# Optimization experiments

Measured on AMD Instinct MI355X. Metric: run time of the kernel, lower is better.

## Reference

```python
import jax, jax.numpy as jnp
import numpy as np
from jax import lax

P_COARSE, P_FINE = 8, 4
EMBED_DIM = 128


def _patchify(x, p):
    # torch unfold(kernel=p, stride=p) then transpose: [B, Hp*Wp, C*p*p]
    B, C, H, W = x.shape
    Hp, Wp = H // p, W // p
    t = x.reshape(B, C, Hp, p, Wp, p).transpose(0, 2, 4, 1, 3, 5)
    return t.reshape(B, Hp * Wp, C * p * p), Hp, Wp


def _edge_map(x):
    gray = x.mean(axis=1, keepdims=True)
    kx = jnp.array([[-1., 0., 1.], [-2., 0., 2.], [-1., 0., 1.]], gray.dtype)[None, None]
    ky = jnp.array([[-1., -2., -1.], [0., 0., 0.], [1., 2., 1.]], gray.dtype)[None, None]
    pad = [(1, 1), (1, 1)]
    sx = lax.conv_general_dilated(gray, kx, (1, 1), pad)
    sy = lax.conv_general_dilated(gray, ky, (1, 1), pad)
    e = jnp.sqrt(sx * sx + sy * sy)
    B, _, H, W = e.shape
    # avg_pool2d(4, stride=4)
    return e.reshape(B, 1, H // 4, 4, W // 4, 4).mean(axis=(3, 5))


def _compact(tok, m):
    # stream-compact masked rows to the front, zero-pad the rest (pad_sequence semantics, padded to full Nf)
    Nf, D = tok.shape
    pos = jnp.cumsum(m) - 1
    pos = jnp.where(m, pos, Nf)  # unmasked rows go to overflow slot
    out = jnp.zeros((Nf + 1, D), tok.dtype).at[pos].set(tok)
    return out[:Nf]


def setup_inputs() -> dict:
    key = jax.random.key(0)
    ks = jax.random.split(key, 6)
    D = EMBED_DIM
    pd_c = 1 * P_COARSE * P_COARSE
    pd_f = 1 * P_FINE * P_FINE
    return {
        "x": jax.random.normal(ks[0], (8, 1, 512, 512), jnp.float32),
        "w_coarse": jax.random.normal(ks[1], (pd_c, D), jnp.float32) / np.sqrt(pd_c),
        "b_coarse": jnp.zeros((D,), jnp.float32),
        "w_fine": jax.random.normal(ks[2], (pd_f, D), jnp.float32) / np.sqrt(pd_f),
        "b_fine": jnp.zeros((D,), jnp.float32),
        "type_emb": jax.random.normal(ks[3], (2, D), jnp.float32) * 0.02,
    }


def reference(x, w_coarse, b_coarse, w_fine, b_fine, type_emb):
    B = x.shape[0]
    # coarse branch
    pc, Hc, Wc = _patchify(x, P_COARSE)
    coarse = pc @ w_coarse + b_coarse + type_emb[0]  # [B, Nc, D]
    # edge-driven mask
    edges = _edge_map(x)  # [B,1,He,We]
    mask = edges > edges.mean(axis=(2, 3), keepdims=True)
    # fine branch
    pf, Hf, Wf = _patchify(x, P_FINE)
    fine = pf @ w_fine + b_fine  # [B, Nf, D]
    # nearest upsample mask to (Hf, Wf): integer factor repeat
    m = mask[:, 0]
    m = jnp.repeat(jnp.repeat(m, Hf // m.shape[1], axis=1), Wf // m.shape[2], axis=2)
    mask_flat = m.reshape(B, -1)  # [B, Nf]
    fine_c = jax.vmap(_compact)(fine, mask_flat) + type_emb[1]
    tokens = jnp.concatenate([coarse, fine_c], axis=1)
    return tokens, mask_flat
```

## Files before the change

kernel.cpp:

```cpp
#include <hip/hip_runtime.h>

#define IMH 512
#define IMW 512
#define BATCH 8
#define NTOK 20480
#define NC 4096
#define NF 16384
#define ED 128

__global__ __launch_bounds__(256) void edge_kernel(const float* __restrict__ x,
                                                   double* __restrict__ edges) {
    int b = blockIdx.z;
    int ty0 = blockIdx.y * 64;
    int tx0 = blockIdx.x * 64;
    __shared__ float sm[66][68];
    const float* img = x + (size_t)b * (IMH * IMW);
    for (int idx = threadIdx.x; idx < 66 * 66; idx += 256) {
        int r = idx / 66, c = idx - r * 66;
        int gy = ty0 - 1 + r, gx = tx0 - 1 + c;
        float v = 0.f;
        if (gy >= 0 && gy < IMH && gx >= 0 && gx < IMW) v = img[gy * IMW + gx];
        sm[r][c] = v;
    }
    __syncthreads();
    int t = threadIdx.x;
    int cy = t >> 4, cx = t & 15;
    double acc = 0.0;
    #pragma unroll
    for (int dy = 0; dy < 4; ++dy) {
        int py = cy * 4 + dy + 1;
        #pragma unroll
        for (int dx = 0; dx < 4; ++dx) {
            int px = cx * 4 + dx + 1;
            double a00 = (double)sm[py - 1][px - 1];
            double a01 = (double)sm[py - 1][px];
            double a02 = (double)sm[py - 1][px + 1];
            double a10 = (double)sm[py][px - 1];
            double a12 = (double)sm[py][px + 1];
            double a20 = (double)sm[py + 1][px - 1];
            double a21 = (double)sm[py + 1][px];
            double a22 = (double)sm[py + 1][px + 1];
            double sx = (a02 + 2.0 * a12 + a22) - (a00 + 2.0 * a10 + a20);
            double sy = (a20 + 2.0 * a21 + a22) - (a00 + 2.0 * a01 + a02);
            acc += sqrt(sx * sx + sy * sy);
        }
    }
    int gy = (ty0 >> 2) + cy;
    int gx = (tx0 >> 2) + cx;
    edges[((size_t)b << 14) + gy * 128 + gx] = acc * (1.0 / 16.0);
}

__global__ __launch_bounds__(1024) void scan_kernel(const double* __restrict__ edges,
                                                    int* __restrict__ pos,
                                                    int* __restrict__ Karr,
                                                    float* __restrict__ mask_out) {
    int b = blockIdx.x;
    const double* e = edges + ((size_t)b << 14);
    int t = threadIdx.x;
    double v[16];
    double s = 0.0;
    #pragma unroll
    for (int j = 0; j < 16; ++j) { v[j] = e[t * 16 + j]; s += v[j]; }
    __shared__ double red[1024];
    red[t] = s;
    __syncthreads();
    for (int off = 512; off > 0; off >>= 1) {
        if (t < off) red[t] += red[t + off];
        __syncthreads();
    }
    double mean = red[0] * (1.0 / 16384.0);
    int m[16];
    int cnt = 0;
    #pragma unroll
    for (int j = 0; j < 16; ++j) { m[j] = (v[j] > mean) ? 1 : 0; cnt += m[j]; }
    __shared__ int sc[1024];
    sc[t] = cnt;
    __syncthreads();
    for (int off = 1; off < 1024; off <<= 1) {
        int add = (t >= off) ? sc[t - off] : 0;
        __syncthreads();
        sc[t] += add;
        __syncthreads();
    }
    int excl = sc[t] - cnt;
    int K = sc[1023];
    int run = excl;
    #pragma unroll
    for (int j = 0; j < 16; ++j) {
        int i = t * 16 + j;
        mask_out[((size_t)b << 14) + i] = m[j] ? 1.0f : 0.0f;
        pos[((size_t)b << 14) + i] = m[j] ? run : -1;
        run += m[j];
    }
    if (t == 0) Karr[b] = K;
}

__global__ __launch_bounds__(128) void coarse_kernel(const float* __restrict__ x,
                                                     const float* __restrict__ wc,
                                                     const float* __restrict__ bc,
                                                     const float* __restrict__ temb,
                                                     float* __restrict__ out) {
    int b = blockIdx.y;
    int p0 = blockIdx.x * 8;
    int hp = p0 >> 6;
    int wp0 = p0 & 63;
    int d = threadIdx.x;
    float wcol[64];
    #pragma unroll
    for (int k = 0; k < 64; ++k) wcol[k] = wc[k * ED + d];
    __shared__ float sm[8][64];
    const float* img = x + ((size_t)b * IMH + hp * 8) * IMW + wp0 * 8;
    #pragma unroll
    for (int idx = d; idx < 512; idx += 128) {
        int r = idx >> 6, c = idx & 63;
        sm[r][c] = img[r * IMW + c];
    }
    __syncthreads();
    float base = bc[d] + temb[d];
    #pragma unroll
    for (int p = 0; p < 8; ++p) {
        float acc = base;
        #pragma unroll
        for (int k = 0; k < 64; ++k) {
            acc += sm[k >> 3][p * 8 + (k & 7)] * wcol[k];
        }
        out[((size_t)b * NTOK + (p0 + p)) * ED + d] = acc;
    }
}

__global__ __launch_bounds__(128) void fine_kernel(const float* __restrict__ x,
                                                   const float* __restrict__ wf,
                                                   const float* __restrict__ bf,
                                                   const float* __restrict__ temb,
                                                   const int* __restrict__ pos,
                                                   const int* __restrict__ Karr,
                                                   float* __restrict__ out) {
    int b = blockIdx.y;
    int i0 = blockIdx.x * 16;
    int hf = i0 >> 7;
    int wf0 = i0 & 127;
    int d = threadIdx.x;
    float wcol[16];
    #pragma unroll
    for (int k = 0; k < 16; ++k) wcol[k] = wf[k * ED + d];
    __shared__ float sm[4][64];
    const float* img = x + ((size_t)b * IMH + hf * 4) * IMW + wf0 * 4;
    #pragma unroll
    for (int idx = d; idx < 256; idx += 128) {
        int r = idx >> 6, c = idx & 63;
        sm[r][c] = img[r * IMW + c];
    }
    __syncthreads();
    int K = Karr[b];
    float fill = temb[ED + d];
    float base = bf[d] + fill;
    float* tok = out + ((size_t)b * NTOK + NC) * ED;
    #pragma unroll
    for (int p = 0; p < 16; ++p) {
        int i = i0 + p;
        int ps = pos[((size_t)b << 14) + i];
        if (ps >= 0) {
            float acc = base;
            #pragma unroll
            for (int k = 0; k < 16; ++k) {
                acc += sm[k >> 2][p * 4 + (k & 3)] * wcol[k];
            }
            tok[(size_t)ps * ED + d] = acc;
        }
        if (i >= K) {
            tok[(size_t)i * ED + d] = fill;
        }
    }
}

extern "C" void kernel_launch(void* const* d_in, const int* in_sizes, int n_in,
                              void* d_out, int out_size, void* d_ws, size_t ws_size,
                              hipStream_t stream) {
    const float* x    = (const float*)d_in[0];
    const float* wc   = (const float*)d_in[1];
    const float* bc   = (const float*)d_in[2];
    const float* wfp  = (const float*)d_in[3];
    const float* bfp  = (const float*)d_in[4];
    const float* temb = (const float*)d_in[5];
    float* out = (float*)d_out;

    double* edges = (double*)d_ws;
    int* pos  = (int*)((char*)d_ws + (size_t)BATCH * NF * sizeof(double));
    int* Karr = (int*)((char*)d_ws + (size_t)BATCH * NF * (sizeof(double) + sizeof(int)));

    float* mask_out = out + (size_t)BATCH * NTOK * ED;

    edge_kernel<<<dim3(8, 8, 8), 256, 0, stream>>>(x, edges);
    scan_kernel<<<dim3(BATCH), 1024, 0, stream>>>(edges, pos, Karr, mask_out);
    coarse_kernel<<<dim3(512, BATCH), 128, 0, stream>>>(x, wc, bc, temb, out);
    fine_kernel<<<dim3(1024, BATCH), 128, 0, stream>>>(x, wfp, bfp, temb, pos, Karr, out);
}
```

Before: 56.95 us.

## Fuse edge and coarse kernels, use wave-shuffle scan, vectorize fine projection

Merges the edge-map and coarse-projection kernels into one launch whose blocks branch by index and share a union of shared memory. The coarse path stages its outputs in shared memory and writes them with float4 stores. The scan kernel replaces its shared-memory tree reduction and scan with wave shuffles plus a 16-entry cross-wave step, and writes its results as vectors. The fine kernel gives each thread four output channels via float4 weights and stores. Together these aim to cut launch count, barrier overhead and store transactions, at the cost of more registers per thread and a mixed-branch launch.

```diff
diff --git a/kernel.cpp b/kernel.cpp
--- a/kernel.cpp
+++ b/kernel.cpp
@@ -8,46 +8,101 @@
 #define NF 16384
 #define ED 128
 
-__global__ __launch_bounds__(256) void edge_kernel(const float* __restrict__ x,
-                                                   double* __restrict__ edges) {
-    int b = blockIdx.z;
-    int ty0 = blockIdx.y * 64;
-    int tx0 = blockIdx.x * 64;
-    __shared__ float sm[66][68];
-    const float* img = x + (size_t)b * (IMH * IMW);
-    for (int idx = threadIdx.x; idx < 66 * 66; idx += 256) {
-        int r = idx / 66, c = idx - r * 66;
-        int gy = ty0 - 1 + r, gx = tx0 - 1 + c;
-        float v = 0.f;
-        if (gy >= 0 && gy < IMH && gx >= 0 && gx < IMW) v = img[gy * IMW + gx];
-        sm[r][c] = v;
-    }
-    __syncthreads();
+__global__ __launch_bounds__(256) void fused_edge_coarse(const float* __restrict__ x,
+                                                         const float* __restrict__ wc,
+                                                         const float* __restrict__ bc,
+                                                         const float* __restrict__ temb,
+                                                         float* __restrict__ out,
+                                                         double* __restrict__ edges) {
+    __shared__ union {
+        float esm[66][68];
+        struct { float smc[8][128]; float smo[16][128]; } c;
+    } U;
+    int blk = blockIdx.x;
     int t = threadIdx.x;
-    int cy = t >> 4, cx = t & 15;
-    double acc = 0.0;
-    #pragma unroll
-    for (int dy = 0; dy < 4; ++dy) {
-        int py = cy * 4 + dy + 1;
-        #pragma unroll
-        for (int dx = 0; dx < 4; ++dx) {
-            int px = cx * 4 + dx + 1;
-            double a00 = (double)sm[py - 1][px - 1];
-            double a01 = (double)sm[py - 1][px];
-            double a02 = (double)sm[py - 1][px + 1];
-            double a10 = (double)sm[py][px - 1];
-            double a12 = (double)sm[py][px + 1];
-            double a20 = (double)sm[py + 1][px - 1];
-            double a21 = (double)sm[py + 1][px];
-            double a22 = (double)sm[py + 1][px + 1];
-            double sx = (a02 + 2.0 * a12 + a22) - (a00 + 2.0 * a10 + a20);
-            double sy = (a20 + 2.0 * a21 + a22) - (a00 + 2.0 * a01 + a02);
-            acc += sqrt(sx * sx + sy * sy);
-        }
-    }
-    int gy = (ty0 >> 2) + cy;
-    int gx = (tx0 >> 2) + cx;
-    edges[((size_t)b << 14) + gy * 128 + gx] = acc * (1.0 / 16.0);
+    if (blk < 2048) {
+        int b = blk >> 8;
+        int p0 = (blk & 255) * 16;
+        int hp = p0 >> 6;
+        int wp0 = p0 & 63;
+        int d = t & 127;
+        int h = t >> 7;
+        float wcol[64];
+        #pragma unroll
+        for (int k = 0; k < 64; ++k) wcol[k] = wc[k * ED + d];
+        const float* img = x + ((size_t)b * IMH + hp * 8) * IMW + wp0 * 8;
+        {
+            int r = t >> 5, c4 = t & 31;
+            *(float4*)&U.c.smc[r][c4 * 4] = *(const float4*)&img[r * IMW + c4 * 4];
+        }
+        __syncthreads();
+        float base = bc[d] + temb[d];
+        float accs[8];
+        #pragma unroll
+        for (int p = 0; p < 8; ++p) {
+            int col0 = h * 64 + p * 8;
+            float acc = base;
+            #pragma unroll
+            for (int r = 0; r < 8; ++r) {
+                float4 v0 = *(const float4*)&U.c.smc[r][col0];
+                float4 v1 = *(const float4*)&U.c.smc[r][col0 + 4];
+                acc += v0.x * wcol[r * 8 + 0] + v0.y * wcol[r * 8 + 1]
+                     + v0.z * wcol[r * 8 + 2] + v0.w * wcol[r * 8 + 3]
+                     + v1.x * wcol[r * 8 + 4] + v1.y * wcol[r * 8 + 5]
+                     + v1.z * wcol[r * 8 + 6] + v1.w * wcol[r * 8 + 7];
+            }
+            accs[p] = acc;
+        }
+        #pragma unroll
+        for (int p = 0; p < 8; ++p) U.c.smo[h * 8 + p][d] = accs[p];
+        __syncthreads();
+        float* dst = out + ((size_t)b * NTOK + p0) * ED;
+        const float* so = (const float*)U.c.smo;
+        #pragma unroll
+        for (int j = 0; j < 2; ++j) {
+            int i = t + 256 * j;
+            *(float4*)&dst[i * 4] = *(const float4*)&so[i * 4];
+        }
+    } else {
+        int blk2 = blk - 2048;
+        int b = blk2 >> 6;
+        int tile = blk2 & 63;
+        int ty0 = (tile >> 3) * 64;
+        int tx0 = (tile & 7) * 64;
+        const float* img = x + (size_t)b * (IMH * IMW);
+        for (int idx = t; idx < 66 * 66; idx += 256) {
+            int r = idx / 66, c = idx - r * 66;
+            int gy = ty0 - 1 + r, gx = tx0 - 1 + c;
+            float v = 0.f;
+            if (gy >= 0 && gy < IMH && gx >= 0 && gx < IMW) v = img[gy * IMW + gx];
+            U.esm[r][c] = v;
+        }
+        __syncthreads();
+        int cy = t >> 4, cx = t & 15;
+        double acc = 0.0;
+        #pragma unroll
+        for (int dy = 0; dy < 4; ++dy) {
+            int py = cy * 4 + dy + 1;
+            #pragma unroll
+            for (int dx = 0; dx < 4; ++dx) {
+                int px = cx * 4 + dx + 1;
+                double a00 = (double)U.esm[py - 1][px - 1];
+                double a01 = (double)U.esm[py - 1][px];
+                double a02 = (double)U.esm[py - 1][px + 1];
+                double a10 = (double)U.esm[py][px - 1];
+                double a12 = (double)U.esm[py][px + 1];
+                double a20 = (double)U.esm[py + 1][px - 1];
+                double a21 = (double)U.esm[py + 1][px];
+                double a22 = (double)U.esm[py + 1][px + 1];
+                double sx = (a02 + 2.0 * a12 + a22) - (a00 + 2.0 * a10 + a20);
+                double sy = (a20 + 2.0 * a21 + a22) - (a00 + 2.0 * a01 + a02);
+                acc += sqrt(sx * sx + sy * sy);
+            }
+        }
+        int gy = (ty0 >> 2) + cy;
+        int gx = (tx0 >> 2) + cx;
+        edges[((size_t)b << 14) + gy * 128 + gx] = acc * (1.0 / 16.0);
+    }
 }
 
 __global__ __launch_bounds__(1024) void scan_kernel(const double* __restrict__ edges,
@@ -57,118 +112,107 @@
     int b = blockIdx.x;
     const double* e = edges + ((size_t)b << 14);
     int t = threadIdx.x;
+    int lane = t & 63, wid = t >> 6;
     double v[16];
+    #pragma unroll
+    for (int j = 0; j < 8; ++j) {
+        double2 dv = *(const double2*)&e[t * 16 + j * 2];
+        v[2 * j] = dv.x; v[2 * j + 1] = dv.y;
+    }
     double s = 0.0;
     #pragma unroll
-    for (int j = 0; j < 16; ++j) { v[j] = e[t * 16 + j]; s += v[j]; }
-    __shared__ double red[1024];
-    red[t] = s;
+    for (int j = 0; j < 16; ++j) s += v[j];
+    #pragma unroll
+    for (int off = 32; off > 0; off >>= 1) s += __shfl_xor(s, off);
+    __shared__ double wsum[16];
+    __shared__ int wcnt[16];
+    if (lane == 0) wsum[wid] = s;
     __syncthreads();
-    for (int off = 512; off > 0; off >>= 1) {
-        if (t < off) red[t] += red[t + off];
-        __syncthreads();
-    }
-    double mean = red[0] * (1.0 / 16384.0);
-    int m[16];
-    int cnt = 0;
+    double total = 0.0;
+    #pragma unroll
+    for (int w = 0; w < 16; ++w) total += wsum[w];
+    double mean = total * (1.0 / 16384.0);
+    int m[16], cnt = 0;
     #pragma unroll
     for (int j = 0; j < 16; ++j) { m[j] = (v[j] > mean) ? 1 : 0; cnt += m[j]; }
-    __shared__ int sc[1024];
-    sc[t] = cnt;
+    int incl = cnt;
+    #pragma unroll
+    for (int off = 1; off < 64; off <<= 1) {
+        int up = __shfl_up(incl, off);
+        if (lane >= off) incl += up;
+    }
+    if (lane == 63) wcnt[wid] = incl;
     __syncthreads();
-    for (int off = 1; off < 1024; off <<= 1) {
-        int add = (t >= off) ? sc[t - off] : 0;
-        __syncthreads();
-        sc[t] += add;
-        __syncthreads();
-    }
-    int excl = sc[t] - cnt;
-    int K = sc[1023];
-    int run = excl;
+    int woff = 0, Ktot = 0;
+    #pragma unroll
+    for (int w = 0; w < 16; ++w) { int c = wcnt[w]; Ktot += c; if (w < wid) woff += c; }
+    int run = woff + incl - cnt;
+    float mf[16]; int pv[16];
     #pragma unroll
     for (int j = 0; j < 16; ++j) {
-        int i = t * 16 + j;
-        mask_out[((size_t)b << 14) + i] = m[j] ? 1.0f : 0.0f;
-        pos[((size_t)b << 14) + i] = m[j] ? run : -1;
+        pv[j] = m[j] ? run : -1;
         run += m[j];
-    }
-    if (t == 0) Karr[b] = K;
-}
-
-__global__ __launch_bounds__(128) void coarse_kernel(const float* __restrict__ x,
-                                                     const float* __restrict__ wc,
-                                                     const float* __restrict__ bc,
-                                                     const float* __restrict__ temb,
-                                                     float* __restrict__ out) {
-    int b = blockIdx.y;
-    int p0 = blockIdx.x * 8;
-    int hp = p0 >> 6;
-    int wp0 = p0 & 63;
-    int d = threadIdx.x;
-    float wcol[64];
-    #pragma unroll
-    for (int k = 0; k < 64; ++k) wcol[k] = wc[k * ED + d];
-    __shared__ float sm[8][64];
-    const float* img = x + ((size_t)b * IMH + hp * 8) * IMW + wp0 * 8;
-    #pragma unroll
-    for (int idx = d; idx < 512; idx += 128) {
-        int r = idx >> 6, c = idx & 63;
-        sm[r][c] = img[r * IMW + c];
-    }
-    __syncthreads();
-    float base = bc[d] + temb[d];
-    #pragma unroll
-    for (int p = 0; p < 8; ++p) {
-        float acc = base;
-        #pragma unroll
-        for (int k = 0; k < 64; ++k) {
-            acc += sm[k >> 3][p * 8 + (k & 7)] * wcol[k];
-        }
-        out[((size_t)b * NTOK + (p0 + p)) * ED + d] = acc;
-    }
-}
-
-__global__ __launch_bounds__(128) void fine_kernel(const float* __restrict__ x,
-                                                   const float* __restrict__ wf,
-                                                   const float* __restrict__ bf,
+        mf[j] = m[j] ? 1.0f : 0.0f;
+    }
+    float* mb = mask_out + ((size_t)b << 14) + t * 16;
+    int* pb = pos + ((size_t)b << 14) + t * 16;
+    #pragma unroll
+    for (int q = 0; q < 4; ++q) {
+        *(float4*)&mb[q * 4] = make_float4(mf[4 * q], mf[4 * q + 1], mf[4 * q + 2], mf[4 * q + 3]);
+        *(int4*)&pb[q * 4] = make_int4(pv[4 * q], pv[4 * q + 1], pv[4 * q + 2], pv[4 * q + 3]);
+    }
+    if (t == 0) Karr[b] = Ktot;
+}
+
+__global__ __launch_bounds__(256) void fine_kernel(const float* __restrict__ x,
+                                                   const float* __restrict__ wfp,
+                                                   const float* __restrict__ bfp,
                                                    const float* __restrict__ temb,
                                                    const int* __restrict__ pos,
                                                    const int* __restrict__ Karr,
                                                    float* __restrict__ out) {
     int b = blockIdx.y;
-    int i0 = blockIdx.x * 16;
+    int i0 = blockIdx.x * 32;
     int hf = i0 >> 7;
     int wf0 = i0 & 127;
-    int d = threadIdx.x;
-    float wcol[16];
-    #pragma unroll
-    for (int k = 0; k < 16; ++k) wcol[k] = wf[k * ED + d];
-    __shared__ float sm[4][64];
+    int t = threadIdx.x;
+    int d4 = t & 31;
+    int g = t >> 5;
+    __shared__ float smx[4][128];
+    float4 wcol[16];
+    #pragma unroll
+    for (int k = 0; k < 16; ++k) wcol[k] = *(const float4*)&wfp[k * ED + d4 * 4];
     const float* img = x + ((size_t)b * IMH + hf * 4) * IMW + wf0 * 4;
-    #pragma unroll
-    for (int idx = d; idx < 256; idx += 128) {
-        int r = idx >> 6, c = idx & 63;
-        sm[r][c] = img[r * IMW + c];
+    if (t < 128) {
+        int r = t >> 5, c4 = t & 31;
+        *(float4*)&smx[r][c4 * 4] = *(const float4*)&img[r * IMW + c4 * 4];
     }
     __syncthreads();
     int K = Karr[b];
-    float fill = temb[ED + d];
-    float base = bf[d] + fill;
-    float* tok = out + ((size_t)b * NTOK + NC) * ED;
-    #pragma unroll
-    for (int p = 0; p < 16; ++p) {
+    const int* posb = pos + ((size_t)b << 14);
+    float4 fill = *(const float4*)&temb[ED + d4 * 4];
+    float4 bse = *(const float4*)&bfp[d4 * 4];
+    float4 base = make_float4(bse.x + fill.x, bse.y + fill.y, bse.z + fill.z, bse.w + fill.w);
+    float4* tok = (float4*)(out + ((size_t)b * NTOK + NC) * ED);
+    #pragma unroll
+    for (int pp = 0; pp < 4; ++pp) {
+        int p = g + pp * 8;
         int i = i0 + p;
-        int ps = pos[((size_t)b << 14) + i];
+        int ps = posb[i];
         if (ps >= 0) {
-            float acc = base;
+            float4 acc = base;
             #pragma unroll
-            for (int k = 0; k < 16; ++k) {
-                acc += sm[k >> 2][p * 4 + (k & 3)] * wcol[k];
+            for (int r = 0; r < 4; ++r) {
+                float4 vv = *(const float4*)&smx[r][p * 4];
+                acc.x += vv.x * wcol[4 * r].x + vv.y * wcol[4 * r + 1].x + vv.z * wcol[4 * r + 2].x + vv.w * wcol[4 * r + 3].x;
+                acc.y += vv.x * wcol[4 * r].y + vv.y * wcol[4 * r + 1].y + vv.z * wcol[4 * r + 2].y + vv.w * wcol[4 * r + 3].y;
+                acc.z += vv.x * wcol[4 * r].z + vv.y * wcol[4 * r + 1].z + vv.z * wcol[4 * r + 2].z + vv.w * wcol[4 * r + 3].z;
+                acc.w += vv.x * wcol[4 * r].w + vv.y * wcol[4 * r + 1].w + vv.z * wcol[4 * r + 2].w + vv.w * wcol[4 * r + 3].w;
             }
-            tok[(size_t)ps * ED + d] = acc;
+            tok[(size_t)ps * 32 + d4] = acc;
         }
         if (i >= K) {
-            tok[(size_t)i * ED + d] = fill;
+            tok[(size_t)i * 32 + d4] = fill;
         }
     }
 }
@@ -190,8 +234,7 @@
 
     float* mask_out = out + (size_t)BATCH * NTOK * ED;
 
-    edge_kernel<<<dim3(8, 8, 8), 256, 0, stream>>>(x, edges);
+    fused_edge_coarse<<<dim3(2560), 256, 0, stream>>>(x, wc, bc, temb, out, edges);
     scan_kernel<<<dim3(BATCH), 1024, 0, stream>>>(edges, pos, Karr, mask_out);
-    coarse_kernel<<<dim3(512, BATCH), 128, 0, stream>>>(x, wc, bc, temb, out);
-    fine_kernel<<<dim3(1024, BATCH), 128, 0, stream>>>(x, wfp, bfp, temb, pos, Karr, out);
-}
+    fine_kernel<<<dim3(512, BATCH), 256, 0, stream>>>(x, wfp, bfp, temb, pos, Karr, out);
+}
```

Result: slower. 58.18 us (+2.2%).
